# Performance work log

Hardware: AMD Instinct MI355X
Metric: run time of the kernel (lower is better)

The kernel has to match this reference:

```python
import jax, jax.numpy as jnp
import numpy as np

DIM = 256
HEADS = 8
WSZ = (2, 7, 7)
SSZ = (1, 3, 3)
EPS = 1e-5


def _rel_index(wsz):
    wt, wh, ww = wsz
    coords = np.stack(np.meshgrid(np.arange(wt), np.arange(wh), np.arange(ww), indexing='ij'))
    coords = coords.reshape(3, -1)  # (3, N)
    rel = coords[:, :, None] - coords[:, None, :]  # (3, N, N)
    rel = rel.transpose(1, 2, 0).copy()  # (N, N, 3)
    rel[:, :, 0] += wt - 1
    rel[:, :, 1] += wh - 1
    rel[:, :, 2] += ww - 1
    rel[:, :, 0] *= (2 * wh - 1) * (2 * ww - 1)
    rel[:, :, 1] *= (2 * ww - 1)
    return rel.sum(-1)  # (N, N) int


def _attn_mask_np(T, H, W, wsz, ssz):
    wt, wh, ww = wsz
    st, sh, sw = ssz
    img = np.zeros((T, H, W), np.int32)
    cnt = 0
    for t in (slice(0, -wt), slice(-wt, -st), slice(-st, None)):
        for h in (slice(0, -wh), slice(-wh, -sh), slice(-sh, None)):
            for w in (slice(0, -ww), slice(-ww, -sw), slice(-sw, None)):
                img[t, h, w] = cnt
                cnt += 1
    m = img.reshape(T // wt, wt, H // wh, wh, W // ww, ww)
    m = m.transpose(0, 2, 4, 1, 3, 5).reshape(-1, wt * wh * ww)  # (nW, N)
    diff = m[:, :, None] - m[:, None, :]
    return np.where(diff != 0, -100.0, 0.0).astype(np.float32)  # (nW, N, N)


def _ln(x, w, b):
    mu = x.mean(-1, keepdims=True)
    var = jnp.mean((x - mu) ** 2, -1, keepdims=True)
    return (x - mu) * jax.lax.rsqrt(var + EPS) * w + b


def _window_partition(x, wsz):
    B, T, H, W, C = x.shape
    wt, wh, ww = wsz
    x = x.reshape(B, T // wt, wt, H // wh, wh, W // ww, ww, C)
    x = x.transpose(0, 1, 3, 5, 2, 4, 6, 7)
    return x.reshape(-1, wt * wh * ww, C)


def _window_reverse(xw, wsz, B, T, H, W):
    wt, wh, ww = wsz
    C = xw.shape[-1]
    x = xw.reshape(B, T // wt, H // wh, W // ww, wt, wh, ww, C)
    x = x.transpose(0, 1, 4, 2, 5, 3, 6, 7)
    return x.reshape(B, T, H, W, C)


def setup_inputs() -> dict:
    key = jax.random.key(0)
    ks = jax.random.split(key, 8)
    B, T, H, W = 2, 8, 56, 56
    d = DIM
    hid = 4 * d
    rpe_rows = (2 * WSZ[0] - 1) * (2 * WSZ[1] - 1) * (2 * WSZ[2] - 1)
    s = 0.02
    return {
        'x': jax.random.normal(ks[0], (B, T, H, W, d), jnp.float32),
        'norm1_w': jnp.ones((d,), jnp.float32),
        'norm1_b': jnp.zeros((d,), jnp.float32),
        'qkv_w': jax.random.normal(ks[1], (3 * d, d), jnp.float32) * s,
        'qkv_b': jnp.zeros((3 * d,), jnp.float32),
        'proj_w': jax.random.normal(ks[2], (d, d), jnp.float32) * s,
        'proj_b': jnp.zeros((d,), jnp.float32),
        'rpe_table': jax.random.normal(ks[3], (rpe_rows, HEADS), jnp.float32) * s,
        'norm2_w': jnp.ones((d,), jnp.float32),
        'norm2_b': jnp.zeros((d,), jnp.float32),
        'fc1_w': jax.random.normal(ks[4], (hid, d), jnp.float32) * s,
        'fc1_b': jnp.zeros((hid,), jnp.float32),
        'fc2_w': jax.random.normal(ks[5], (d, hid), jnp.float32) * s,
        'fc2_b': jnp.zeros((d,), jnp.float32),
    }


def reference(x, norm1_w, norm1_b, qkv_w, qkv_b, proj_w, proj_b, rpe_table,
              norm2_w, norm2_b, fc1_w, fc1_b, fc2_w, fc2_b):
    B, T, H, W, C = x.shape
    wt, wh, ww = WSZ
    N = wt * wh * ww
    hd = C // HEADS
    scale = hd ** -0.5

    shortcut = x
    h = _ln(x, norm1_w, norm1_b)
    # shifted branch: cyclic roll + mask
    h = jnp.roll(h, (-SSZ[0], -SSZ[1], -SSZ[2]), axis=(1, 2, 3))
    mask = jnp.asarray(_attn_mask_np(T, H, W, WSZ, SSZ))  # (nW, N, N)
    nW = mask.shape[0]

    xw = _window_partition(h, WSZ)  # (B*nW, N, C)
    Bw = xw.shape[0]

    qkv = xw @ qkv_w.T + qkv_b  # (Bw, N, 3C)
    qkv = qkv.reshape(Bw, N, 3, HEADS, hd).transpose(2, 0, 3, 1, 4)
    q, k, v = qkv[0], qkv[1], qkv[2]  # (Bw, H, N, hd)

    idx = _rel_index(WSZ)  # (N, N)
    bias = rpe_table[idx].transpose(2, 0, 1)  # (heads, N, N)

    attn = jnp.einsum('bhnd,bhmd->bhnm', q * scale, k) + bias[None]
    attn = attn.reshape(B, nW, HEADS, N, N) + mask[None, :, None]
    attn = jax.nn.softmax(attn, axis=-1).reshape(Bw, HEADS, N, N)

    out = jnp.einsum('bhnm,bhmd->bhnd', attn, v)
    out = out.transpose(0, 2, 1, 3).reshape(Bw, N, C)
    out = out @ proj_w.T + proj_b

    out = _window_reverse(out, WSZ, B, T, H, W)
    out = jnp.roll(out, (SSZ[0], SSZ[1], SSZ[2]), axis=(1, 2, 3))

    x = shortcut + out
    h2 = _ln(x, norm2_w, norm2_b)
    h2 = jax.nn.gelu(h2 @ fc1_w.T + fc1_b, approximate=False)
    h2 = h2 @ fc2_w.T + fc2_b
    return x + h2
```

## Files before the change

kernel.cpp:

```cpp
#include <hip/hip_runtime.h>
#include <math.h>

#define TOKENS 50176
#define NWIN   512
#define C_DIM  256

typedef __attribute__((ext_vector_type(8))) short short8;
typedef __attribute__((ext_vector_type(4))) float f32x4;

__device__ __forceinline__ unsigned short f2bf(float f) {
    unsigned int u = __builtin_bit_cast(unsigned int, f);
    u += 0x7fffu + ((u >> 16) & 1);
    return (unsigned short)(u >> 16);
}

__device__ __forceinline__ void gll16(const void* g, void* l) {
    __builtin_amdgcn_global_load_lds(
        (const __attribute__((address_space(1))) unsigned int*)g,
        (__attribute__((address_space(3))) unsigned int*)l, 16, 0, 0);
}

__device__ __forceinline__ int win_token_to_flat(int u) {
    int g = u / 98;
    int n = u - g * 98;
    int bb  = g >> 8;
    int rem = g & 255;
    int tb = rem >> 6, hb = (rem >> 3) & 7, wb = rem & 7;
    int dt = n / 49;
    int r2 = n - dt * 49;
    int dh = r2 / 7, dw = r2 - dh * 7;
    int t = tb * 2 + dt, h = hb * 7 + dh, w = wb * 7 + dw;
    int ts = (t + 1) & 7;
    int hs = h + 3; if (hs >= 56) hs -= 56;
    int wsx = w + 3; if (wsx >= 56) wsx -= 56;
    return ((bb * 8 + ts) * 56 + hs) * 56 + wsx;
}

__global__ __launch_bounds__(256) void cvt_kernel(
        const float* __restrict__ src, unsigned short* __restrict__ dst, int n) {
    int i = blockIdx.x * 256 + threadIdx.x;
    if (i < n) dst[i] = f2bf(src[i]);
}

__global__ __launch_bounds__(256) void bm_kernel(
        const float* __restrict__ rpe, float* __restrict__ bm) {
    int i = blockIdx.x * 256 + threadIdx.x;
    int c  = i % 112;
    int t1 = i / 112;
    int r  = t1 % 112;
    int t2 = t1 / 112;
    int head = t2 & 7;
    int cls  = t2 >> 3;
    float val;
    if (c >= 98) {
        val = -1e30f;
    } else if (r >= 98) {
        val = 0.f;
    } else {
        int dt = r / 49, rr = r - dt * 49, dh = rr / 7, dw = rr - dh * 7;
        int dt2 = c / 49, cc = c - dt2 * 49, dh2 = cc / 7, dw2 = cc - dh2 * 7;
        int rt  = (cls & 4) ? (dt  == 0 ? 1 : 2) : 0;
        int rh  = (cls & 2) ? (dh  <  4 ? 1 : 2) : 0;
        int rw  = (cls & 1) ? (dw  <  4 ? 1 : 2) : 0;
        int rt2 = (cls & 4) ? (dt2 == 0 ? 1 : 2) : 0;
        int rh2 = (cls & 2) ? (dh2 <  4 ? 1 : 2) : 0;
        int rw2 = (cls & 1) ? (dw2 <  4 ? 1 : 2) : 0;
        int reg1 = rt * 9 + rh * 3 + rw, reg2 = rt2 * 9 + rh2 * 3 + rw2;
        int idx = (dt - dt2 + 1) * 169 + (dh - dh2 + 6) * 13 + (dw - dw2 + 6);
        val = rpe[idx * 8 + head] + ((reg1 == reg2) ? 0.f : -100.f);
    }
    bm[i] = val;
}

template<bool GATHER>
__global__ __launch_bounds__(256) void ln_kernel(
        const float* __restrict__ x, const float* __restrict__ w,
        const float* __restrict__ b, unsigned short* __restrict__ out) {
    int token = blockIdx.x * 4 + (threadIdx.x >> 6);
    int lane  = threadIdx.x & 63;
    size_t so = GATHER ? (size_t)win_token_to_flat(token) * C_DIM
                       : (size_t)token * C_DIM;
    const float* src = x + so;
    float v[4];
    float sum = 0.f;
#pragma unroll
    for (int j = 0; j < 4; ++j) { v[j] = src[lane + 64 * j]; sum += v[j]; }
#pragma unroll
    for (int o = 32; o > 0; o >>= 1) sum += __shfl_xor(sum, o, 64);
    float mu = sum * (1.f / 256.f);
    float var = 0.f;
#pragma unroll
    for (int j = 0; j < 4; ++j) { float d = v[j] - mu; var += d * d; }
#pragma unroll
    for (int o = 32; o > 0; o >>= 1) var += __shfl_xor(var, o, 64);
    float rstd = rsqrtf(var * (1.f / 256.f) + 1e-5f);
    unsigned short* dst = out + (size_t)token * C_DIM;
#pragma unroll
    for (int j = 0; j < 4; ++j) {
        int c = lane + 64 * j;
        dst[c] = f2bf((v[j] - mu) * rstd * w[c] + b[c]);
    }
}

template<int EPI>
__global__ __launch_bounds__(256) void mfma_gemm(
        const unsigned short* __restrict__ A, const unsigned short* __restrict__ B,
        const float* __restrict__ bias, const float* __restrict__ res,
        void* __restrict__ Cout, int M, int N, int K) {
    __shared__ __attribute__((aligned(16))) unsigned short Asm[128 * 32];
    __shared__ __attribute__((aligned(16))) unsigned short Bsm[128 * 32];
    int tid = threadIdx.x;
    int wave = tid >> 6, lane = tid & 63;
    int row0 = blockIdx.y * 128, col0 = blockIdx.x * 128;
    int wr = (wave >> 1) * 64;
    int wc = (wave & 1) * 64;

    f32x4 acc[4][4] = {};

    int sr = tid >> 2;
    int sk = (tid & 3) * 8;
    const unsigned short* Ag0 = A + (size_t)(row0 + sr) * K + sk;
    const unsigned short* Ag1 = A + (size_t)(row0 + 64 + sr) * K + sk;
    const unsigned short* Bg0 = B + (size_t)(col0 + sr) * K + sk;
    const unsigned short* Bg1 = B + (size_t)(col0 + 64 + sr) * K + sk;
    unsigned short* Al = Asm + tid * 8;
    unsigned short* Bl = Bsm + tid * 8;

    int fm = lane & 15, fk = (lane >> 4) * 8;

    for (int k0 = 0; k0 < K; k0 += 32) {
        __syncthreads();
        gll16(Ag0 + k0, Al);
        gll16(Ag1 + k0, Al + 64 * 32);
        gll16(Bg0 + k0, Bl);
        gll16(Bg1 + k0, Bl + 64 * 32);
        __syncthreads();
        short8 af[4], bf[4];
#pragma unroll
        for (int t4 = 0; t4 < 4; ++t4) {
            af[t4] = *(const short8*)&Asm[(wr + t4 * 16 + fm) * 32 + fk];
            bf[t4] = *(const short8*)&Bsm[(wc + t4 * 16 + fm) * 32 + fk];
        }
#pragma unroll
        for (int i = 0; i < 4; ++i)
#pragma unroll
            for (int j = 0; j < 4; ++j)
                acc[i][j] = __builtin_amdgcn_mfma_f32_16x16x32_bf16(
                    af[i], bf[j], acc[i][j], 0, 0, 0);
    }

    int crow0 = row0 + wr + (lane >> 4) * 4;
    int ccol0 = col0 + wc + (lane & 15);
    float bj[4];
#pragma unroll
    for (int j = 0; j < 4; ++j) bj[j] = bias[ccol0 + j * 16];

    if (EPI == 0) {
        unsigned short* C = (unsigned short*)Cout;
        float mul = (col0 < 256) ? 0.17677669529663687f : 1.f;
#pragma unroll
        for (int i = 0; i < 4; ++i)
#pragma unroll
            for (int v = 0; v < 4; ++v) {
                size_t base = (size_t)(crow0 + i * 16 + v) * N + ccol0;
#pragma unroll
                for (int j = 0; j < 4; ++j)
                    C[base + j * 16] = f2bf((acc[i][j][v] + bj[j]) * mul);
            }
    } else if (EPI == 1) {
        float* C = (float*)Cout;
#pragma unroll
        for (int i = 0; i < 4; ++i)
#pragma unroll
            for (int v = 0; v < 4; ++v) {
                int r = crow0 + i * 16 + v;
                size_t base = (size_t)win_token_to_flat(r) * C_DIM + ccol0;
#pragma unroll
                for (int j = 0; j < 4; ++j)
                    C[base + j * 16] = res[base + j * 16] + acc[i][j][v] + bj[j];
            }
    } else if (EPI == 2) {
        unsigned short* C = (unsigned short*)Cout;
#pragma unroll
        for (int i = 0; i < 4; ++i)
#pragma unroll
            for (int v = 0; v < 4; ++v) {
                size_t base = (size_t)(crow0 + i * 16 + v) * N + ccol0;
#pragma unroll
                for (int j = 0; j < 4; ++j) {
                    float val = acc[i][j][v] + bj[j];
                    C[base + j * 16] =
                        f2bf(0.5f * val * (1.f + erff(val * 0.70710678118654752f)));
                }
            }
    } else {
        float* C = (float*)Cout;
#pragma unroll
        for (int i = 0; i < 4; ++i)
#pragma unroll
            for (int v = 0; v < 4; ++v) {
                size_t base = (size_t)(crow0 + i * 16 + v) * N + ccol0;
#pragma unroll
                for (int j = 0; j < 4; ++j)
                    C[base + j * 16] = res[base + j * 16] + acc[i][j][v] + bj[j];
            }
    }
}

__global__ __launch_bounds__(256) void attn_mfma_kernel(
        const unsigned short* __restrict__ qkv, const float* __restrict__ bm,
        unsigned short* __restrict__ out) {
    __shared__ __attribute__((aligned(16))) unsigned short Vt[32][136];
    __shared__ __attribute__((aligned(16))) unsigned short Pw[4][16][136];
    int blk = blockIdx.x;
    int g = blk >> 3, head = blk & 7;
    int tid = threadIdx.x, wave = tid >> 6, lane = tid & 63;

    for (int i = tid; i < 32 * 30; i += 256) {
        int d = i / 30, c = 98 + (i - d * 30);
        Vt[d][c] = 0;
    }
    const unsigned short* vbase = qkv + (size_t)g * 98 * 768 + 512 + head * 32;
    for (int i = tid; i < 98 * 16; i += 256) {
        int n = i >> 4, dp = i & 15;
        unsigned int val = *(const unsigned int*)(vbase + (size_t)n * 768 + dp * 2);
        Vt[dp * 2][n]     = (unsigned short)val;
        Vt[dp * 2 + 1][n] = (unsigned short)(val >> 16);
    }
    {
        int m = lane >> 2, c = 112 + (lane & 3) * 4;
        *(unsigned long long*)&Pw[wave][m][c] = 0ULL;
    }
    __syncthreads();

    const unsigned short* qbase = qkv + (size_t)g * 98 * 768 + head * 32;
    const unsigned short* kbase = qbase + 256;
    int rem = g & 255;
    int cls = (((rem >> 6) == 3) << 2) | (((((rem >> 3) & 7)) == 7) << 1) | ((rem & 7) == 7);
    const float* bmh = bm + (size_t)(cls * 8 + head) * 112 * 112;

    int fm = lane & 15, fq = lane >> 4;
    int fk = fq * 8;
    unsigned short* obase = out + (size_t)g * 98 * 256 + head * 32;

    for (int s = wave; s < 7; s += 4) {
        int m0 = s * 16;
        int arow = m0 + fm; if (arow > 97) arow = 97;
        short8 af = *(const short8*)(qbase + (size_t)arow * 768 + fk);
        f32x4 S[7];
        f32x4 z = {0.f, 0.f, 0.f, 0.f};
#pragma unroll
        for (int j = 0; j < 7; ++j) {
            int krow = j * 16 + fm; if (krow > 97) krow = 97;
            short8 kf = *(const short8*)(kbase + (size_t)krow * 768 + fk);
            S[j] = __builtin_amdgcn_mfma_f32_16x16x32_bf16(af, kf, z, 0, 0, 0);
        }
        const float* bmrow = bmh + (m0 + fq * 4) * 112 + fm;
#pragma unroll
        for (int j = 0; j < 7; ++j)
#pragma unroll
            for (int v = 0; v < 4; ++v)
                S[j][v] += bmrow[v * 112 + j * 16];
        float inv[4];
#pragma unroll
        for (int v = 0; v < 4; ++v) {
            float m_ = S[0][v];
#pragma unroll
            for (int j = 1; j < 7; ++j) m_ = fmaxf(m_, S[j][v]);
#pragma unroll
            for (int o = 1; o < 16; o <<= 1) m_ = fmaxf(m_, __shfl_xor(m_, o, 64));
            float t = 0.f;
#pragma unroll
            for (int j = 0; j < 7; ++j) { S[j][v] = __expf(S[j][v] - m_); t += S[j][v]; }
#pragma unroll
            for (int o = 1; o < 16; o <<= 1) t += __shfl_xor(t, o, 64);
            inv[v] = 1.f / t;
        }
#pragma unroll
        for (int j = 0; j < 7; ++j)
#pragma unroll
            for (int v = 0; v < 4; ++v)
                Pw[wave][fq * 4 + v][j * 16 + fm] = f2bf(S[j][v]);
        f32x4 O0 = {0.f, 0.f, 0.f, 0.f}, O1 = {0.f, 0.f, 0.f, 0.f};
#pragma unroll
        for (int ks = 0; ks < 4; ++ks) {
            short8 pf = *(const short8*)&Pw[wave][fm][ks * 32 + fk];
            short8 v0 = *(const short8*)&Vt[fm][ks * 32 + fk];
            short8 v1 = *(const short8*)&Vt[16 + fm][ks * 32 + fk];
            O0 = __builtin_amdgcn_mfma_f32_16x16x32_bf16(pf, v0, O0, 0, 0, 0);
            O1 = __builtin_amdgcn_mfma_f32_16x16x32_bf16(pf, v1, O1, 0, 0, 0);
        }
#pragma unroll
        for (int v = 0; v < 4; ++v) {
            int row = m0 + fq * 4 + v;
            if (row < 98) {
                obase[(size_t)row * 256 + fm]      = f2bf(O0[v] * inv[v]);
                obase[(size_t)row * 256 + 16 + fm] = f2bf(O1[v] * inv[v]);
            }
        }
    }
}

extern "C" void kernel_launch(void* const* d_in, const int* in_sizes, int n_in,
                              void* d_out, int out_size, void* d_ws, size_t ws_size,
                              hipStream_t stream) {
    const float* x     = (const float*)d_in[0];
    const float* n1w   = (const float*)d_in[1];
    const float* n1b   = (const float*)d_in[2];
    const float* qkvw  = (const float*)d_in[3];
    const float* qkvb  = (const float*)d_in[4];
    const float* projw = (const float*)d_in[5];
    const float* projb = (const float*)d_in[6];
    const float* rpe   = (const float*)d_in[7];
    const float* n2w   = (const float*)d_in[8];
    const float* n2b   = (const float*)d_in[9];
    const float* fc1w  = (const float*)d_in[10];
    const float* fc1b  = (const float*)d_in[11];
    const float* fc2w  = (const float*)d_in[12];
    const float* fc2b  = (const float*)d_in[13];
    float* out = (float*)d_out;

    unsigned short* wqkv  = (unsigned short*)d_ws;
    unsigned short* wproj = wqkv + 768 * 256;
    unsigned short* wfc1  = wproj + 256 * 256;
    unsigned short* wfc2  = wfc1 + 1024 * 256;
    float* bm = (float*)(wfc2 + 256 * 1024);
    unsigned short* actA  = (unsigned short*)(bm + 8 * 8 * 112 * 112);
    unsigned short* attnO = actA + (size_t)TOKENS * 256;
    unsigned short* qkv_bf = attnO + (size_t)TOKENS * 256;
    unsigned short* fc1o = qkv_bf;

    bm_kernel<<<8 * 8 * 112 * 112 / 256, 256, 0, stream>>>(rpe, bm);
    cvt_kernel<<<(768 * 256 + 255) / 256, 256, 0, stream>>>(qkvw, wqkv, 768 * 256);
    cvt_kernel<<<(256 * 256 + 255) / 256, 256, 0, stream>>>(projw, wproj, 256 * 256);
    cvt_kernel<<<(1024 * 256 + 255) / 256, 256, 0, stream>>>(fc1w, wfc1, 1024 * 256);
    cvt_kernel<<<(256 * 1024 + 255) / 256, 256, 0, stream>>>(fc2w, wfc2, 256 * 1024);

    ln_kernel<true><<<TOKENS / 4, 256, 0, stream>>>(x, n1w, n1b, actA);
    mfma_gemm<0><<<dim3(768 / 128, TOKENS / 128), 256, 0, stream>>>(
        actA, wqkv, qkvb, nullptr, qkv_bf, TOKENS, 768, 256);
    attn_mfma_kernel<<<NWIN * 8, 256, 0, stream>>>(qkv_bf, bm, attnO);
    mfma_gemm<1><<<dim3(256 / 128, TOKENS / 128), 256, 0, stream>>>(
        attnO, wproj, projb, x, out, TOKENS, 256, 256);
    ln_kernel<false><<<TOKENS / 4, 256, 0, stream>>>(out, n2w, n2b, actA);
    mfma_gemm<2><<<dim3(1024 / 128, TOKENS / 128), 256, 0, stream>>>(
        actA, wfc1, fc1b, nullptr, fc1o, TOKENS, 1024, 256);
    mfma_gemm<3><<<dim3(256 / 128, TOKENS / 128), 256, 0, stream>>>(
        fc1o, wfc2, fc2b, out, out, TOKENS, 256, 1024);
}
```

Measured before the change: 407.7 us.

## Fuse LayerNorm into QKV and FC1 GEMMs; add dedicated full-width FC2 kernel

Replaces the standalone LayerNorm kernels with a fused ln_gemm kernel. It normalizes a 64-row tile into swizzled LDS, keeps the A fragments in registers, and streams 64-column weight chunks over the full K=256. This removes the bf16 activation round trip through global memory and two launches. FC2 becomes its own kernel that computes all 256 output columns per 64-row tile, so the fc1 output is read only once, with XOR-swizzled LDS layouts. The trade-offs are that the fused kernels fetch weights serially with no double buffering, use 64KB of LDS which may limit occupancy, and give each wave a smaller tile.

```diff
diff --git a/kernel.cpp b/kernel.cpp
--- a/kernel.cpp
+++ b/kernel.cpp
@@ -3,7 +3,6 @@
 
 #define TOKENS 50176
 #define NWIN   512
-#define C_DIM  256
 
 typedef __attribute__((ext_vector_type(8))) short short8;
 typedef __attribute__((ext_vector_type(4))) float f32x4;
@@ -72,41 +71,169 @@
     bm[i] = val;
 }
 
-template<bool GATHER>
-__global__ __launch_bounds__(256) void ln_kernel(
-        const float* __restrict__ x, const float* __restrict__ w,
-        const float* __restrict__ b, unsigned short* __restrict__ out) {
-    int token = blockIdx.x * 4 + (threadIdx.x >> 6);
-    int lane  = threadIdx.x & 63;
-    size_t so = GATHER ? (size_t)win_token_to_flat(token) * C_DIM
-                       : (size_t)token * C_DIM;
-    const float* src = x + so;
-    float v[4];
-    float sum = 0.f;
-#pragma unroll
-    for (int j = 0; j < 4; ++j) { v[j] = src[lane + 64 * j]; sum += v[j]; }
-#pragma unroll
-    for (int o = 32; o > 0; o >>= 1) sum += __shfl_xor(sum, o, 64);
-    float mu = sum * (1.f / 256.f);
-    float var = 0.f;
-#pragma unroll
-    for (int j = 0; j < 4; ++j) { float d = v[j] - mu; var += d * d; }
-#pragma unroll
-    for (int o = 32; o > 0; o >>= 1) var += __shfl_xor(var, o, 64);
-    float rstd = rsqrtf(var * (1.f / 256.f) + 1e-5f);
-    unsigned short* dst = out + (size_t)token * C_DIM;
-#pragma unroll
-    for (int j = 0; j < 4; ++j) {
-        int c = lane + 64 * j;
-        dst[c] = f2bf((v[j] - mu) * rstd * w[c] + b[c]);
-    }
-}
-
-template<int EPI>
-__global__ __launch_bounds__(256) void mfma_gemm(
+template<int NCOLS, int EPI, bool GATHER>
+__global__ __launch_bounds__(256) void ln_gemm_kernel(
+        const float* __restrict__ X, const float* __restrict__ lnw,
+        const float* __restrict__ lnb, const unsigned short* __restrict__ W,
+        const float* __restrict__ bias, unsigned short* __restrict__ out) {
+    __shared__ __attribute__((aligned(16))) unsigned short h[64 * 256];
+    __shared__ __attribute__((aligned(16))) unsigned short wbuf[64 * 256];
+    int tid = threadIdx.x, wave = tid >> 6, lane = tid & 63;
+    int row0 = blockIdx.x * 64;
+
+    float4 gw = *(const float4*)(lnw + lane * 4);
+    float4 gb = *(const float4*)(lnb + lane * 4);
+    for (int t = 0; t < 16; ++t) {
+        int row = wave * 16 + t;
+        int token = row0 + row;
+        size_t src = GATHER ? (size_t)win_token_to_flat(token) * 256
+                            : (size_t)token * 256;
+        float4 v = *(const float4*)(X + src + lane * 4);
+        float sum = v.x + v.y + v.z + v.w;
+#pragma unroll
+        for (int o = 32; o > 0; o >>= 1) sum += __shfl_xor(sum, o, 64);
+        float mu = sum * (1.f / 256.f);
+        float d0 = v.x - mu, d1 = v.y - mu, d2 = v.z - mu, d3 = v.w - mu;
+        float var = d0 * d0 + d1 * d1 + d2 * d2 + d3 * d3;
+#pragma unroll
+        for (int o = 32; o > 0; o >>= 1) var += __shfl_xor(var, o, 64);
+        float rstd = rsqrtf(var * (1.f / 256.f) + 1e-5f);
+        unsigned long long pk =
+              (unsigned long long)f2bf(d0 * rstd * gw.x + gb.x)
+            | ((unsigned long long)f2bf(d1 * rstd * gw.y + gb.y) << 16)
+            | ((unsigned long long)f2bf(d2 * rstd * gw.z + gb.z) << 32)
+            | ((unsigned long long)f2bf(d3 * rstd * gw.w + gb.w) << 48);
+        int cp = (lane >> 1) ^ (row & 7);
+        *(unsigned long long*)&h[row * 256 + cp * 8 + (lane & 1) * 4] = pk;
+    }
+
+    int fm = lane & 15, fq = lane >> 4;
+    int arow = wave * 16 + fm;
+    short8 af[8];
+#pragma unroll
+    for (int kw = 0; kw < 8; ++kw) {
+        int c = (kw * 4 + fq) ^ (arow & 7);
+        af[kw] = *(const short8*)&h[arow * 256 + c * 8];
+    }
+
+    const float qscale = 0.17677669529663687f;
+    for (int nc = 0; nc < NCOLS / 64; ++nc) {
+        __syncthreads();
+#pragma unroll
+        for (int i = 0; i < 8; ++i) {
+            int s = tid + 256 * i;
+            int wrow = s >> 5, cp = s & 31;
+            int c = cp ^ (wrow & 7);
+            gll16(W + (size_t)(nc * 64 + wrow) * 256 + c * 8, wbuf + s * 8);
+        }
+        __syncthreads();
+        f32x4 acc[4] = {};
+#pragma unroll
+        for (int nt = 0; nt < 4; ++nt) {
+            int brow = nt * 16 + fm;
+#pragma unroll
+            for (int kw = 0; kw < 8; ++kw) {
+                int c = (kw * 4 + fq) ^ (brow & 7);
+                short8 bfr = *(const short8*)&wbuf[brow * 256 + c * 8];
+                acc[nt] = __builtin_amdgcn_mfma_f32_16x16x32_bf16(
+                    af[kw], bfr, acc[nt], 0, 0, 0);
+            }
+        }
+#pragma unroll
+        for (int nt = 0; nt < 4; ++nt) {
+            int col = nc * 64 + nt * 16 + fm;
+            float b = bias[col];
+            size_t obase = (size_t)(row0 + wave * 16 + fq * 4) * NCOLS + col;
+#pragma unroll
+            for (int v = 0; v < 4; ++v) {
+                float val = acc[nt][v] + b;
+                if (EPI == 0)
+                    val *= (nc < 4) ? qscale : 1.f;
+                else
+                    val = 0.5f * val * (1.f + erff(val * 0.70710678118654752f));
+                out[obase + (size_t)v * NCOLS] = f2bf(val);
+            }
+        }
+    }
+}
+
+__global__ __launch_bounds__(256) void fc2_kernel(
+        const unsigned short* __restrict__ A, const unsigned short* __restrict__ W,
+        const float* __restrict__ bias, const float* __restrict__ res,
+        float* __restrict__ out) {
+    __shared__ __attribute__((aligned(16))) unsigned short As[64 * 32];
+    __shared__ __attribute__((aligned(16))) unsigned short Bs[256 * 32];
+    int tid = threadIdx.x, wave = tid >> 6, lane = tid & 63;
+    int fm = lane & 15, fq = lane >> 4;
+    int row0 = blockIdx.x * 64;
+
+    f32x4 acc[4][4] = {};
+
+    int apair = tid >> 3, aidx = tid & 7;
+    int aig = aidx ^ (apair & 7);
+    const unsigned short* Asrc =
+        A + (size_t)(row0 + apair * 2 + (aig >> 2)) * 1024 + (aig & 3) * 8;
+
+    int bslots[4];
+    const unsigned short* Bsrc[4];
+#pragma unroll
+    for (int i = 0; i < 4; ++i) {
+        int s = tid + 256 * i;
+        int pr = s >> 3, idx = s & 7;
+        int ig = idx ^ (pr & 7);
+        bslots[i] = s;
+        Bsrc[i] = W + (size_t)(pr * 2 + (ig >> 2)) * 1024 + (ig & 3) * 8;
+    }
+
+    for (int k0 = 0; k0 < 1024; k0 += 32) {
+        __syncthreads();
+        gll16(Asrc + k0, As + tid * 8);
+#pragma unroll
+        for (int i = 0; i < 4; ++i)
+            gll16(Bsrc[i] + k0, Bs + bslots[i] * 8);
+        __syncthreads();
+        short8 afr[4], bfr[4];
+#pragma unroll
+        for (int mt = 0; mt < 4; ++mt) {
+            int r = mt * 16 + fm;
+            int idx = (((r & 1) << 2) | fq) ^ ((r >> 1) & 7);
+            afr[mt] = *(const short8*)&As[((r >> 1) * 8 + idx) * 8];
+        }
+#pragma unroll
+        for (int nt = 0; nt < 4; ++nt) {
+            int r = wave * 64 + nt * 16 + fm;
+            int idx = (((r & 1) << 2) | fq) ^ ((r >> 1) & 7);
+            bfr[nt] = *(const short8*)&Bs[((r >> 1) * 8 + idx) * 8];
+        }
+#pragma unroll
+        for (int mt = 0; mt < 4; ++mt)
+#pragma unroll
+            for (int nt = 0; nt < 4; ++nt)
+                acc[mt][nt] = __builtin_amdgcn_mfma_f32_16x16x32_bf16(
+                    afr[mt], bfr[nt], acc[mt][nt], 0, 0, 0);
+    }
+
+#pragma unroll
+    for (int nt = 0; nt < 4; ++nt) {
+        int col = wave * 64 + nt * 16 + fm;
+        float b = bias[col];
+#pragma unroll
+        for (int mt = 0; mt < 4; ++mt) {
+            size_t base = (size_t)(row0 + mt * 16 + fq * 4) * 256 + col;
+#pragma unroll
+            for (int v = 0; v < 4; ++v) {
+                size_t off = base + (size_t)v * 256;
+                out[off] = res[off] + acc[mt][nt][v] + b;
+            }
+        }
+    }
+}
+
+__global__ __launch_bounds__(256) void proj_gemm(
         const unsigned short* __restrict__ A, const unsigned short* __restrict__ B,
         const float* __restrict__ bias, const float* __restrict__ res,
-        void* __restrict__ Cout, int M, int N, int K) {
+        float* __restrict__ C) {
+    const int N = 256, K = 256;
     __shared__ __attribute__((aligned(16))) unsigned short Asm[128 * 32];
     __shared__ __attribute__((aligned(16))) unsigned short Bsm[128 * 32];
     int tid = threadIdx.x;
@@ -155,56 +282,16 @@
 #pragma unroll
     for (int j = 0; j < 4; ++j) bj[j] = bias[ccol0 + j * 16];
 
-    if (EPI == 0) {
-        unsigned short* C = (unsigned short*)Cout;
-        float mul = (col0 < 256) ? 0.17677669529663687f : 1.f;
-#pragma unroll
-        for (int i = 0; i < 4; ++i)
-#pragma unroll
-            for (int v = 0; v < 4; ++v) {
-                size_t base = (size_t)(crow0 + i * 16 + v) * N + ccol0;
-#pragma unroll
-                for (int j = 0; j < 4; ++j)
-                    C[base + j * 16] = f2bf((acc[i][j][v] + bj[j]) * mul);
-            }
-    } else if (EPI == 1) {
-        float* C = (float*)Cout;
-#pragma unroll
-        for (int i = 0; i < 4; ++i)
-#pragma unroll
-            for (int v = 0; v < 4; ++v) {
-                int r = crow0 + i * 16 + v;
-                size_t base = (size_t)win_token_to_flat(r) * C_DIM + ccol0;
-#pragma unroll
-                for (int j = 0; j < 4; ++j)
-                    C[base + j * 16] = res[base + j * 16] + acc[i][j][v] + bj[j];
-            }
-    } else if (EPI == 2) {
-        unsigned short* C = (unsigned short*)Cout;
-#pragma unroll
-        for (int i = 0; i < 4; ++i)
-#pragma unroll
-            for (int v = 0; v < 4; ++v) {
-                size_t base = (size_t)(crow0 + i * 16 + v) * N + ccol0;
-#pragma unroll
-                for (int j = 0; j < 4; ++j) {
-                    float val = acc[i][j][v] + bj[j];
-                    C[base + j * 16] =
-                        f2bf(0.5f * val * (1.f + erff(val * 0.70710678118654752f)));
-                }
-            }
-    } else {
-        float* C = (float*)Cout;
-#pragma unroll
-        for (int i = 0; i < 4; ++i)
-#pragma unroll
-            for (int v = 0; v < 4; ++v) {
-                size_t base = (size_t)(crow0 + i * 16 + v) * N + ccol0;
-#pragma unroll
-                for (int j = 0; j < 4; ++j)
-                    C[base + j * 16] = res[base + j * 16] + acc[i][j][v] + bj[j];
-            }
-    }
+#pragma unroll
+    for (int i = 0; i < 4; ++i)
+#pragma unroll
+        for (int v = 0; v < 4; ++v) {
+            int r = crow0 + i * 16 + v;
+            size_t base = (size_t)win_token_to_flat(r) * 256 + ccol0;
+#pragma unroll
+            for (int j = 0; j < 4; ++j)
+                C[base + j * 16] = res[base + j * 16] + acc[i][j][v] + bj[j];
+        }
 }
 
 __global__ __launch_bounds__(256) void attn_mfma_kernel(
@@ -325,8 +412,7 @@
     unsigned short* wfc1  = wproj + 256 * 256;
     unsigned short* wfc2  = wfc1 + 1024 * 256;
     float* bm = (float*)(wfc2 + 256 * 1024);
-    unsigned short* actA  = (unsigned short*)(bm + 8 * 8 * 112 * 112);
-    unsigned short* attnO = actA + (size_t)TOKENS * 256;
+    unsigned short* attnO = (unsigned short*)(bm + 8 * 8 * 112 * 112);
     unsigned short* qkv_bf = attnO + (size_t)TOKENS * 256;
     unsigned short* fc1o = qkv_bf;
 
@@ -336,15 +422,12 @@
     cvt_kernel<<<(1024 * 256 + 255) / 256, 256, 0, stream>>>(fc1w, wfc1, 1024 * 256);
     cvt_kernel<<<(256 * 1024 + 255) / 256, 256, 0, stream>>>(fc2w, wfc2, 256 * 1024);
 
-    ln_kernel<true><<<TOKENS / 4, 256, 0, stream>>>(x, n1w, n1b, actA);
-    mfma_gemm<0><<<dim3(768 / 128, TOKENS / 128), 256, 0, stream>>>(
-        actA, wqkv, qkvb, nullptr, qkv_bf, TOKENS, 768, 256);
+    ln_gemm_kernel<768, 0, true><<<TOKENS / 64, 256, 0, stream>>>(
+        x, n1w, n1b, wqkv, qkvb, qkv_bf);
     attn_mfma_kernel<<<NWIN * 8, 256, 0, stream>>>(qkv_bf, bm, attnO);
-    mfma_gemm<1><<<dim3(256 / 128, TOKENS / 128), 256, 0, stream>>>(
-        attnO, wproj, projb, x, out, TOKENS, 256, 256);
-    ln_kernel<false><<<TOKENS / 4, 256, 0, stream>>>(out, n2w, n2b, actA);
-    mfma_gemm<2><<<dim3(1024 / 128, TOKENS / 128), 256, 0, stream>>>(
-        actA, wfc1, fc1b, nullptr, fc1o, TOKENS, 1024, 256);
-    mfma_gemm<3><<<dim3(256 / 128, TOKENS / 128), 256, 0, stream>>>(
-        fc1o, wfc2, fc2b, out, out, TOKENS, 256, 1024);
-}
+    proj_gemm<<<dim3(2, TOKENS / 128), 256, 0, stream>>>(
+        attnO, wproj, projb, x, out);
+    ln_gemm_kernel<1024, 2, false><<<TOKENS / 64, 256, 0, stream>>>(
+        out, n2w, n2b, wfc1, fc1b, fc1o);
+    fc2_kernel<<<TOKENS / 64, 256, 0, stream>>>(fc1o, wfc2, fc2b, out, out);
+}
```

Result: slower. 459.8 us (+12.8%).
